# Kernel optimization log

Measured on AMD Instinct MI355X. Metric: run time of the kernel, lower is better.

Reference implementation:

```python
import math
import jax, jax.numpy as jnp
import numpy as np

T = 4096
D_MODEL = 1024
NUM_HEADS = 16
HEAD_DIM = D_MODEL // NUM_HEADS


def setup_inputs() -> dict:
    key = jax.random.key(0)
    k_x, k_wqkv, k_wproj = jax.random.split(key, 3)
    # match eqx.nn.Linear init scale: U(-1/sqrt(in), 1/sqrt(in)); randn*small works too,
    # but keep magnitudes reasonable so softmax isn't saturated.
    s_in = 1.0 / math.sqrt(D_MODEL)
    x = jax.random.normal(k_x, (T, D_MODEL), dtype=jnp.float32)
    W_qkv = jax.random.normal(k_wqkv, (3 * D_MODEL, D_MODEL), dtype=jnp.float32) * s_in
    b_qkv = jnp.zeros((3 * D_MODEL,), dtype=jnp.float32)
    W_proj = jax.random.normal(k_wproj, (D_MODEL, D_MODEL), dtype=jnp.float32) * s_in
    b_proj = jnp.zeros((D_MODEL,), dtype=jnp.float32)
    return {"x": x, "W_qkv": W_qkv, "b_qkv": b_qkv, "W_proj": W_proj, "b_proj": b_proj}


def reference(x, W_qkv, b_qkv, W_proj, b_proj):
    T_, C = x.shape  # (seq, d_model)
    H, hd = NUM_HEADS, HEAD_DIM
    # c_attn: eqx Linear computes W @ x + b per token -> x @ W.T + b
    qkv = x @ W_qkv.T + b_qkv  # (T, 3C)
    q, k, v = jnp.split(qkv, 3, axis=1)
    # (T, C) -> (H, T, hd)
    q = q.reshape(T_, H, hd).swapaxes(0, 1)
    k = k.reshape(T_, H, hd).swapaxes(0, 1)
    v = v.reshape(T_, H, hd).swapaxes(0, 1)
    scores = jnp.einsum("htd,hsd->hts", q, k) / math.sqrt(hd)  # (H, T, T)
    causal = jnp.tril(jnp.ones((T_, T_), dtype=bool))
    scores = jnp.where(causal, scores, -jnp.inf)
    attn = jax.nn.softmax(scores, axis=-1)
    y = jnp.einsum("hts,hsd->htd", attn, v)  # (H, T, hd)
    y = y.swapaxes(0, 1).reshape(T_, C)
    y = y @ W_proj.T + b_proj
    return y
```

## Files before the change

kernel.cpp:

```cpp
#include <hip/hip_runtime.h>
#include <math.h>
#include <string.h>

#define T_SEQ 4096
#define DM 1024
#define NH 16
#define HD 64

typedef short s8v __attribute__((ext_vector_type(8)));
typedef float f4v __attribute__((ext_vector_type(4)));

__device__ inline unsigned short f2bf(float f) {
    unsigned u; memcpy(&u, &f, 4);
    u = u + 0x7fffu + ((u >> 16) & 1u);
    return (unsigned short)(u >> 16);
}

__device__ inline float bf2f(unsigned short s) {
    unsigned u = (unsigned)s << 16;
    float f; memcpy(&f, &u, 4);
    return f;
}

__device__ inline float exp2fn(float x) {
#if __has_builtin(__builtin_amdgcn_exp2f)
    return __builtin_amdgcn_exp2f(x);
#else
    return exp2f(x);
#endif
}

__device__ inline void gld_lds16(const void* g, void* l) {
    __builtin_amdgcn_global_load_lds(
        (const __attribute__((address_space(1))) void*)g,
        (__attribute__((address_space(3))) void*)l, 16, 0, 0);
}

__global__ __launch_bounds__(256)
void cvt3(const float* __restrict__ i0, unsigned short* __restrict__ o0, int n0,
          const float* __restrict__ i1, unsigned short* __restrict__ o1, int n1,
          const float* __restrict__ i2, unsigned short* __restrict__ o2, int n2) {
    int i = blockIdx.x * 256 + threadIdx.x;
    const float* in; unsigned short* out; int j;
    if (i < n0)           { in = i0; out = o0; j = i; }
    else if (i < n0 + n1) { in = i1; out = o1; j = i - n0; }
    else if (i < n0 + n1 + n2) { in = i2; out = o2; j = i - n0 - n1; }
    else return;
    const float4* p = (const float4*)(in + (size_t)j * 8);
    float4 a = p[0], b = p[1];
    unsigned short o[8] = {f2bf(a.x), f2bf(a.y), f2bf(a.z), f2bf(a.w),
                           f2bf(b.x), f2bf(b.y), f2bf(b.z), f2bf(b.w)};
    uint4 pk; memcpy(&pk, o, 16);
    *(uint4*)(out + (size_t)j * 8) = pk;
}

template<int MODE, int TN>
__global__ __launch_bounds__(256)
void gemm_bt_mfma(const unsigned short* __restrict__ A, const unsigned short* __restrict__ B,
                  const float* __restrict__ bias, void* __restrict__ Cout,
                  unsigned short* __restrict__ qbuf, unsigned short* __restrict__ kbuf2,
                  unsigned short* __restrict__ vT,
                  int M, int N, int K) {
    constexpr int NF = TN / 32;
    __shared__ __align__(16) short As[4096];
    __shared__ __align__(16) short Bs[TN * 32];
    const int tid = threadIdx.x;
    const int w = tid >> 6, lane = tid & 63;
    const int wr = w >> 1, wc = w & 1;
    const int m0 = blockIdx.y * 128, n0 = blockIdx.x * TN;

    const bool doA = (w < 2);
    const bool doStage = doA || ((w & 1) * 64 < TN);
    const unsigned short* src = doA ? A : B;
    const int rbase = (doA ? m0 : n0) + (w & 1) * 64;
    const unsigned short* gsrc = src + (size_t)(rbase + (lane & 15)) * K + ((lane >> 4) * 8);
    short* ldst = (doA ? As : Bs) + ((w & 1) * 4) * 512;

    f4v acc[4][NF];
    #pragma unroll
    for (int i = 0; i < 4; ++i)
        #pragma unroll
        for (int j = 0; j < NF; ++j) acc[i][j] = (f4v){0.f, 0.f, 0.f, 0.f};

    for (int k0 = 0; k0 < K; k0 += 32) {
        __syncthreads();
        if (doStage) {
            #pragma unroll
            for (int i = 0; i < 4; ++i)
                gld_lds16(gsrc + (size_t)(i * 16) * K + k0, ldst + i * 512);
        }
        __syncthreads();

        s8v af[4], bf[NF];
        #pragma unroll
        for (int i = 0; i < 4; ++i) af[i] = *(const s8v*)&As[((wr * 4 + i) * 64 + lane) * 8];
        #pragma unroll
        for (int j = 0; j < NF; ++j) bf[j] = *(const s8v*)&Bs[((wc * NF + j) * 64 + lane) * 8];
        #pragma unroll
        for (int i = 0; i < 4; ++i)
            #pragma unroll
            for (int j = 0; j < NF; ++j)
                acc[i][j] = __builtin_amdgcn_mfma_f32_16x16x32_bf16(af[i], bf[j], acc[i][j], 0, 0, 0);
    }

    const int l15 = lane & 15, quad = lane >> 4;
    float bj[NF];
    #pragma unroll
    for (int j = 0; j < NF; ++j) bj[j] = bias[n0 + wc * (TN / 2) + j * 16 + l15];

    if (MODE == 2 && n0 >= 2 * DM) {
        const int tile = (m0 + wr * 64) >> 6;
        const int hh = ((n0 - 2 * DM) >> 6) + wc;
        #pragma unroll
        for (int i = 0; i < 4; ++i) {
            #pragma unroll
            for (int j = 0; j < NF; ++j) {
                unsigned short o[4];
                #pragma unroll
                for (int rg = 0; rg < 4; ++rg) o[rg] = f2bf(acc[i][j][rg] + bj[j]);
                unsigned long long pk; memcpy(&pk, o, 8);
                size_t off = (size_t)hh * 262144 + (size_t)tile * 4096
                           + (size_t)((j * 2 + (i >> 1)) * 64 + lane) * 8 + (i & 1) * 4;
                *(unsigned long long*)&vT[off] = pk;
            }
        }
    } else if (MODE == 2) {
        unsigned short* dst = (n0 < DM) ? qbuf : kbuf2;
        const int nb = (n0 < DM) ? n0 : n0 - DM;
        #pragma unroll
        for (int i = 0; i < 4; ++i) {
            #pragma unroll
            for (int rg = 0; rg < 4; ++rg) {
                int row = m0 + wr * 64 + i * 16 + quad * 4 + rg;
                #pragma unroll
                for (int j = 0; j < NF; ++j) {
                    int col = nb + wc * (TN / 2) + j * 16 + l15;
                    dst[(size_t)row * DM + col] = f2bf(acc[i][j][rg] + bj[j]);
                }
            }
        }
    } else {
        #pragma unroll
        for (int i = 0; i < 4; ++i) {
            #pragma unroll
            for (int rg = 0; rg < 4; ++rg) {
                int row = m0 + wr * 64 + i * 16 + quad * 4 + rg;
                #pragma unroll
                for (int j = 0; j < NF; ++j) {
                    int col = n0 + wc * (TN / 2) + j * 16 + l15;
                    ((float*)Cout)[(size_t)row * N + col] = acc[i][j][rg] + bj[j];
                }
            }
        }
    }
}

__device__ __forceinline__ void soft_step(f4v* st, bool diag, int qloc, int quad,
                                          float& lr, s8v& pf0, s8v& pf1) {
    const float C2  = 0.1803368851f;
    const float MC2 = 12.0f * 0.1803368851f;
    float sv[4][4];
    #pragma unroll
    for (int kb = 0; kb < 4; ++kb)
        #pragma unroll
        for (int rg = 0; rg < 4; ++rg) {
            float s = st[kb][rg];
            if (diag && (kb * 16 + quad * 4 + rg > qloc)) s = -3.0e38f;
            float t = exp2fn(fmaf(s, C2, -MC2));
            sv[kb][rg] = t;
            lr += t;
        }
    int pk[4][2];
    #pragma unroll
    for (int kb = 0; kb < 4; ++kb) {
        unsigned u0 = __float_as_uint(sv[kb][0]) + 0x8000u;
        unsigned u1 = __float_as_uint(sv[kb][1]) + 0x8000u;
        unsigned u2 = __float_as_uint(sv[kb][2]) + 0x8000u;
        unsigned u3 = __float_as_uint(sv[kb][3]) + 0x8000u;
        pk[kb][0] = (int)__builtin_amdgcn_perm(u1, u0, 0x07060302);
        pk[kb][1] = (int)__builtin_amdgcn_perm(u3, u2, 0x07060302);
    }
    int4 a = {pk[0][0], pk[0][1], pk[1][0], pk[1][1]};
    int4 b = {pk[2][0], pk[2][1], pk[3][0], pk[3][1]};
    memcpy(&pf0, &a, 16);
    memcpy(&pf1, &b, 16);
}

__global__ __launch_bounds__(256, 3)
void attn_mfma7(const unsigned short* __restrict__ qb,
                const unsigned short* __restrict__ kbf,
                const unsigned short* __restrict__ vT,
                unsigned short* __restrict__ y0,
                unsigned short* __restrict__ y1,
                unsigned short* __restrict__ y2,
                float* __restrict__ lsum) {
    const int b = blockIdx.x;
    const int par = b % 3;
    const int idx = b / 3;
    const int h = idx & 15, a = idx >> 4;
    const int tid = threadIdx.x;
    const int w = tid >> 6, lane = tid & 63;
    const int quad = lane >> 4, l15 = lane & 15;
    const int cq = h * HD;
    unsigned short* ypar = (par == 0) ? y0 : (par == 1) ? y1 : y2;
    float* lpar = lsum + ((size_t)par * NH + h) * T_SEQ;
    const unsigned short* vbase = vT + (size_t)h * 262144;

    __shared__ short KB[2][4096];
    __shared__ short VTs[2][4096];
    __shared__ short QB[8192];

    for (int ph = 0; ph < 2; ++ph) {
        const int qt = ph ? (31 - a) : a;
        const int q0 = qt * 128;
        const int kmax = 2 * qt + 1;
        const int nk = (kmax >= par) ? (kmax - par) / 3 + 1 : 0;
        const int kt0 = par * 64;

        __syncthreads();
        #pragma unroll
        for (int rr = 0; rr < 4; ++rr) {
            int ch = rr * 256 + tid;
            int qg = ch >> 7, hf = (ch >> 6) & 1, ln = ch & 63;
            gld_lds16(qb + (size_t)(q0 + qg * 16 + (ln & 15)) * DM + cq + hf * 32 + ((ln >> 4) << 3),
                      &QB[(ch & ~63) * 8]);
        }
        if (nk > 0) {
            #pragma unroll
            for (int rr = 0; rr < 2; ++rr) {
                int ch = rr * 256 + tid;
                int blk = ch >> 7, hf = (ch >> 6) & 1, ln = ch & 63;
                gld_lds16(kbf + (size_t)(kt0 + blk * 16 + (ln & 15)) * DM + cq + hf * 32 + ((ln >> 4) << 3),
                          &KB[0][(ch & ~63) * 8]);
                gld_lds16(vbase + (size_t)(kt0 >> 6) * 4096 + (size_t)ch * 8,
                          &VTs[0][(ch & ~63) * 8]);
            }
        }
        __syncthreads();

        s8v qf[2][2];
        #pragma unroll
        for (int g = 0; g < 2; ++g)
            #pragma unroll
            for (int hf = 0; hf < 2; ++hf)
                qf[g][hf] = *(const s8v*)&QB[((((g * 4 + w) * 2 + hf) * 64) + lane) * 8];

        f4v O0[4], O1[4];
        #pragma unroll
        for (int ob = 0; ob < 4; ++ob) {
            O0[ob] = (f4v){0.f, 0.f, 0.f, 0.f};
            O1[ob] = (f4v){0.f, 0.f, 0.f, 0.f};
        }
        float lr0 = 0.f, lr1 = 0.f;

        for (int i = 0; i < nk; ++i) {
            const int kt = par + 3 * i;
            const int p = i & 1;
            const bool g0a = (kt <= 2 * qt);
            const bool m0 = (kt == 2 * qt);
            const bool m1 = (kt == 2 * qt + 1);
            if (i < nk - 1) {
                const int k1 = kt0 + (i + 1) * 192;
                #pragma unroll
                for (int rr = 0; rr < 2; ++rr) {
                    int ch = rr * 256 + tid;
                    int blk = ch >> 7, hf = (ch >> 6) & 1, ln = ch & 63;
                    gld_lds16(kbf + (size_t)(k1 + blk * 16 + (ln & 15)) * DM + cq
                                  + hf * 32 + ((ln >> 4) << 3),
                              &KB[p ^ 1][(ch & ~63) * 8]);
                    gld_lds16(vbase + (size_t)(k1 >> 6) * 4096 + (size_t)ch * 8,
                              &VTs[p ^ 1][(ch & ~63) * 8]);
                }
            }

            f4v st0[4], st1[4];
            #pragma unroll
            for (int kb = 0; kb < 4; ++kb) {
                s8v k0f = *(const s8v*)&KB[p][((kb * 2 + 0) * 64 + lane) * 8];
                s8v k1f = *(const s8v*)&KB[p][((kb * 2 + 1) * 64 + lane) * 8];
                f4v c1 = (f4v){0.f, 0.f, 0.f, 0.f};
                c1 = __builtin_amdgcn_mfma_f32_16x16x32_bf16(k0f, qf[1][0], c1, 0, 0, 0);
                c1 = __builtin_amdgcn_mfma_f32_16x16x32_bf16(k1f, qf[1][1], c1, 0, 0, 0);
                st1[kb] = c1;
                if (g0a) {
                    f4v c0 = (f4v){0.f, 0.f, 0.f, 0.f};
                    c0 = __builtin_amdgcn_mfma_f32_16x16x32_bf16(k0f, qf[0][0], c0, 0, 0, 0);
                    c0 = __builtin_amdgcn_mfma_f32_16x16x32_bf16(k1f, qf[0][1], c0, 0, 0, 0);
                    st0[kb] = c0;
                }
            }

            s8v pf10, pf11, pf00, pf01;
            soft_step(st1, m1, w * 16 + l15, quad, lr1, pf10, pf11);
            if (g0a) soft_step(st0, m0, w * 16 + l15, quad, lr0, pf00, pf01);

            #pragma unroll
            for (int ob = 0; ob < 4; ++ob) {
                s8v v0f = *(const s8v*)&VTs[p][((ob * 2 + 0) * 64 + lane) * 8];
                s8v v1f = *(const s8v*)&VTs[p][((ob * 2 + 1) * 64 + lane) * 8];
                O1[ob] = __builtin_amdgcn_mfma_f32_16x16x32_bf16(v0f, pf10, O1[ob], 0, 0, 0);
                O1[ob] = __builtin_amdgcn_mfma_f32_16x16x32_bf16(v1f, pf11, O1[ob], 0, 0, 0);
                if (g0a) {
                    O0[ob] = __builtin_amdgcn_mfma_f32_16x16x32_bf16(v0f, pf00, O0[ob], 0, 0, 0);
                    O0[ob] = __builtin_amdgcn_mfma_f32_16x16x32_bf16(v1f, pf01, O0[ob], 0, 0, 0);
                }
            }
            __syncthreads();
        }

        lr0 += __shfl_xor(lr0, 16); lr0 += __shfl_xor(lr0, 32);
        lr1 += __shfl_xor(lr1, 16); lr1 += __shfl_xor(lr1, 32);
        #pragma unroll
        for (int g = 0; g < 2; ++g) {
            const f4v* O = g ? O1 : O0;
            int qrow = q0 + g * 64 + w * 16 + l15;
            size_t ybase = (size_t)qrow * DM + cq;
            #pragma unroll
            for (int ob = 0; ob < 4; ++ob) {
                unsigned short o[4];
                #pragma unroll
                for (int rg = 0; rg < 4; ++rg) o[rg] = f2bf(O[ob][rg]);
                unsigned long long pk; memcpy(&pk, o, 8);
                *(unsigned long long*)&ypar[ybase + ob * 16 + quad * 4] = pk;
            }
            if (quad == 0) lpar[qrow] = g ? lr1 : lr0;
        }
    }
}

__global__ __launch_bounds__(256)
void attn_combine3(const unsigned short* __restrict__ y0,
                   const unsigned short* __restrict__ y1,
                   const unsigned short* __restrict__ y2,
                   const float* __restrict__ lsum,
                   unsigned short* __restrict__ yout) {
    int i = blockIdx.x * 256 + threadIdx.x;
    int t = i >> 7, d8 = i & 127;
    int h = d8 >> 3;
    float l = lsum[(size_t)h * T_SEQ + t]
            + lsum[((size_t)NH + h) * T_SEQ + t]
            + lsum[((size_t)2 * NH + h) * T_SEQ + t];
    float inv = 1.f / l;
    size_t off = (size_t)t * DM + d8 * 8;
    uint4 ua = *(const uint4*)(y0 + off);
    uint4 ub = *(const uint4*)(y1 + off);
    uint4 uc = *(const uint4*)(y2 + off);
    const unsigned short* pa = (const unsigned short*)&ua;
    const unsigned short* pb = (const unsigned short*)&ub;
    const unsigned short* pc = (const unsigned short*)&uc;
    unsigned short o[8];
    #pragma unroll
    for (int k = 0; k < 8; ++k)
        o[k] = f2bf((bf2f(pa[k]) + bf2f(pb[k]) + bf2f(pc[k])) * inv);
    uint4 pk; memcpy(&pk, o, 16);
    *(uint4*)(yout + off) = pk;
}

extern "C" void kernel_launch(void* const* d_in, const int* in_sizes, int n_in,
                              void* d_out, int out_size, void* d_ws, size_t ws_size,
                              hipStream_t stream) {
    const float* x     = (const float*)d_in[0];
    const float* Wqkv  = (const float*)d_in[1];
    const float* bqkv  = (const float*)d_in[2];
    const float* Wproj = (const float*)d_in[3];
    const float* bproj = (const float*)d_in[4];
    float* out = (float*)d_out;

    char* ws = (char*)d_ws;
    unsigned short* qbuf  = (unsigned short*)(ws);
    unsigned short* kbuf  = (unsigned short*)(ws + ( 8u << 20));
    unsigned short* vTb   = (unsigned short*)(ws + (16u << 20));
    unsigned short* yattb = (unsigned short*)(ws + (24u << 20));
    unsigned short* wprjb = (unsigned short*)(ws + (32u << 20));
    float*          lsum  = (float*)         (ws + (34u << 20));
    unsigned short* xb    = (unsigned short*)(ws + (35u << 20));
    unsigned short* wqkvb = (unsigned short*)(ws + (43u << 20));
    unsigned short* y0p   = (unsigned short*)(ws + (35u << 20));
    unsigned short* y1p   = (unsigned short*)(ws + (43u << 20));
    unsigned short* y2p   = (unsigned short*)(ws + (51u << 20));

    dim3 blk(256);
    {
        int n0 = T_SEQ * DM / 8, n1 = 3 * DM * DM / 8, n2 = DM * DM / 8;
        cvt3<<<dim3((n0 + n1 + n2 + 255) / 256), blk, 0, stream>>>(
            x, xb, n0, Wqkv, wqkvb, n1, Wproj, wprjb, n2);
    }
    gemm_bt_mfma<2, 128><<<dim3(3 * DM / 128, T_SEQ / 128), blk, 0, stream>>>(
        xb, wqkvb, bqkv, nullptr, qbuf, kbuf, vTb, T_SEQ, 3 * DM, DM);
    attn_mfma7<<<dim3(768), blk, 0, stream>>>(qbuf, kbuf, vTb, y0p, y1p, y2p, lsum);
    attn_combine3<<<dim3(T_SEQ * DM / 8 / 256), blk, 0, stream>>>(y0p, y1p, y2p, lsum, yattb);
    gemm_bt_mfma<0, 64><<<dim3(DM / 64, T_SEQ / 128), blk, 0, stream>>>(
        yattb, wprjb, bproj, out, nullptr, nullptr, nullptr, T_SEQ, DM, DM);
}
```

Baseline: 219.5 us.

## Double-buffer GEMM LDS tiles and remap blocks to XCD-local patches

The GEMM k-loop now uses two LDS buffers, so the next k-slice is loaded while MFMAs run on the current one, and only one barrier is needed per slice. Blocks are launched on a 1D grid and remapped so that each XCD covers a contiguous patch of output tiles, which should improve L2 reuse of the A and B panels. LDS use doubles and the mapping assumes blocks are distributed round-robin across 8 XCDs.

New measurement: 215.7 us. Within noise of the previous version (-1.7%).

```diff
diff --git a/kernel.cpp b/kernel.cpp
--- a/kernel.cpp
+++ b/kernel.cpp
@@ -60,21 +60,27 @@
                   const float* __restrict__ bias, void* __restrict__ Cout,
                   unsigned short* __restrict__ qbuf, unsigned short* __restrict__ kbuf2,
                   unsigned short* __restrict__ vT,
-                  int M, int N, int K) {
+                  int M, int N, int K, int nbx, int patchw, int patchh) {
     constexpr int NF = TN / 32;
-    __shared__ __align__(16) short As[4096];
-    __shared__ __align__(16) short Bs[TN * 32];
+    __shared__ __align__(16) short As[2][4096];
+    __shared__ __align__(16) short Bs[2][TN * 32];
     const int tid = threadIdx.x;
     const int w = tid >> 6, lane = tid & 63;
     const int wr = w >> 1, wc = w & 1;
-    const int m0 = blockIdx.y * 128, n0 = blockIdx.x * TN;
+
+    const int bl = blockIdx.x;
+    const int xcd = bl & 7, ii = bl >> 3;
+    const int pxn = nbx / patchw;
+    const int bx = (xcd % pxn) * patchw + ii % patchw;
+    const int by = (xcd / pxn) * patchh + ii / patchw;
+    const int m0 = by * 128, n0 = bx * TN;
 
     const bool doA = (w < 2);
     const bool doStage = doA || ((w & 1) * 64 < TN);
     const unsigned short* src = doA ? A : B;
     const int rbase = (doA ? m0 : n0) + (w & 1) * 64;
     const unsigned short* gsrc = src + (size_t)(rbase + (lane & 15)) * K + ((lane >> 4) * 8);
-    short* ldst = (doA ? As : Bs) + ((w & 1) * 4) * 512;
+    const int ldoff = ((w & 1) * 4) * 512;
 
     f4v acc[4][NF];
     #pragma unroll
@@ -82,25 +88,34 @@
         #pragma unroll
         for (int j = 0; j < NF; ++j) acc[i][j] = (f4v){0.f, 0.f, 0.f, 0.f};
 
-    for (int k0 = 0; k0 < K; k0 += 32) {
+    auto stage = [&](short* base, int k0) {
+        short* ldst = base + ldoff;
+        #pragma unroll
+        for (int i = 0; i < 4; ++i)
+            gld_lds16(gsrc + (size_t)(i * 16) * K + k0, ldst + i * 512);
+    };
+    auto compute = [&](const short* Ab, const short* Bb) {
+        s8v af[4], bfr[NF];
+        #pragma unroll
+        for (int i = 0; i < 4; ++i) af[i] = *(const s8v*)&Ab[((wr * 4 + i) * 64 + lane) * 8];
+        #pragma unroll
+        for (int j = 0; j < NF; ++j) bfr[j] = *(const s8v*)&Bb[((wc * NF + j) * 64 + lane) * 8];
+        #pragma unroll
+        for (int i = 0; i < 4; ++i)
+            #pragma unroll
+            for (int j = 0; j < NF; ++j)
+                acc[i][j] = __builtin_amdgcn_mfma_f32_16x16x32_bf16(af[i], bfr[j], acc[i][j], 0, 0, 0);
+    };
+
+    if (doStage) stage(doA ? As[0] : Bs[0], 0);
+    __syncthreads();
+    for (int k0 = 0; k0 < K; k0 += 64) {
+        if (doStage) stage(doA ? As[1] : Bs[1], k0 + 32);
+        compute(As[0], Bs[0]);
         __syncthreads();
-        if (doStage) {
-            #pragma unroll
-            for (int i = 0; i < 4; ++i)
-                gld_lds16(gsrc + (size_t)(i * 16) * K + k0, ldst + i * 512);
-        }
+        if (doStage && (k0 + 64 < K)) stage(doA ? As[0] : Bs[0], k0 + 64);
+        compute(As[1], Bs[1]);
         __syncthreads();
-
-        s8v af[4], bf[NF];
-        #pragma unroll
-        for (int i = 0; i < 4; ++i) af[i] = *(const s8v*)&As[((wr * 4 + i) * 64 + lane) * 8];
-        #pragma unroll
-        for (int j = 0; j < NF; ++j) bf[j] = *(const s8v*)&Bs[((wc * NF + j) * 64 + lane) * 8];
-        #pragma unroll
-        for (int i = 0; i < 4; ++i)
-            #pragma unroll
-            for (int j = 0; j < NF; ++j)
-                acc[i][j] = __builtin_amdgcn_mfma_f32_16x16x32_bf16(af[i], bf[j], acc[i][j], 0, 0, 0);
     }
 
     const int l15 = lane & 15, quad = lane >> 4;
@@ -385,10 +400,10 @@
         cvt3<<<dim3((n0 + n1 + n2 + 255) / 256), blk, 0, stream>>>(
             x, xb, n0, Wqkv, wqkvb, n1, Wproj, wprjb, n2);
     }
-    gemm_bt_mfma<2, 128><<<dim3(3 * DM / 128, T_SEQ / 128), blk, 0, stream>>>(
-        xb, wqkvb, bqkv, nullptr, qbuf, kbuf, vTb, T_SEQ, 3 * DM, DM);
+    gemm_bt_mfma<2, 128><<<dim3(768), blk, 0, stream>>>(
+        xb, wqkvb, bqkv, nullptr, qbuf, kbuf, vTb, T_SEQ, 3 * DM, DM, 24, 6, 16);
     attn_mfma7<<<dim3(768), blk, 0, stream>>>(qbuf, kbuf, vTb, y0p, y1p, y2p, lsum);
     attn_combine3<<<dim3(T_SEQ * DM / 8 / 256), blk, 0, stream>>>(y0p, y1p, y2p, lsum, yattb);
-    gemm_bt_mfma<0, 64><<<dim3(DM / 64, T_SEQ / 128), blk, 0, stream>>>(
-        yattb, wprjb, bproj, out, nullptr, nullptr, nullptr, T_SEQ, DM, DM);
-}
+    gemm_bt_mfma<0, 64><<<dim3(512), blk, 0, stream>>>(
+        yattb, wprjb, bproj, out, nullptr, nullptr, nullptr, T_SEQ, DM, DM, 16, 8, 8);
+}
```
